# Kernel tuning notes

Hardware: AMD Instinct MI355X
Metric: run time of the kernel (lower is better)

The kernel has to match this reference:

```python
import jax, jax.numpy as jnp
import numpy as np
from jax import lax

B, C, N = 4, 512, 4096
NH = 8
HD = C // NH          # 64
SR = 2                # sr_ratio
EPS = 1e-5            # BatchNorm eps (torch default)


def setup_inputs() -> dict:
    key = jax.random.key(0)
    ks = jax.random.split(key, 12)
    d = {}
    d["x"] = jax.random.normal(ks[0], (B, C, N), jnp.float32)
    d["y"] = jax.random.normal(ks[1], (B, C, N), jnp.float32)  # unused by forward (faithful to source)
    # Conv1d kernel-size-1 weights == (out_c, in_c) matrices; trunc_normal std=0.02 ~ normal*0.02
    d["Wq"] = jax.random.normal(ks[2], (C, C), jnp.float32) * 0.02
    d["Wk"] = jax.random.normal(ks[3], (C, C), jnp.float32) * 0.02
    # sr: Conv2d(dim, dim, kernel=SR, stride=SR), kaiming-ish init per _init_weights
    fan_out = SR * SR * C
    d["Wsr"] = jax.random.normal(ks[4], (C, C, SR, SR), jnp.float32) * np.sqrt(2.0 / fan_out)
    d["bsr"] = jnp.zeros((C,), jnp.float32)
    # BatchNorm1d(dim) in inference mode
    d["bn_gamma"] = 1.0 + 0.1 * jax.random.normal(ks[5], (C,), jnp.float32)
    d["bn_beta"] = 0.1 * jax.random.normal(ks[6], (C,), jnp.float32)
    d["bn_mean"] = 0.1 * jax.random.normal(ks[7], (C,), jnp.float32)
    d["bn_var"] = 1.0 + 0.1 * jnp.abs(jax.random.normal(ks[8], (C,), jnp.float32))
    d["Wproj"] = jax.random.normal(ks[9], (C, C), jnp.float32) * 0.02
    d["bproj"] = jnp.zeros((C,), jnp.float32)
    d["H"] = 64
    d["W"] = 64
    return d


def reference(x, y, Wq, Wk, Wsr, bsr, bn_gamma, bn_beta, bn_mean, bn_var, Wproj, bproj, H, W):
    scale = HD ** -0.5
    # q: Conv1d(k=1) -> (B,C,N) -> (B,NH,HD,N) -> (B,NH,N,HD)
    q = jnp.einsum('oc,bcn->bon', Wq, x).reshape(B, NH, HD, N).transpose(0, 1, 3, 2)
    # spatial reduction path (sr_ratio > 1): Conv2d stride SR, then BN (inference), then k-proj
    x4 = x.reshape(B, C, H, W)
    xsr = lax.conv_general_dilated(x4, Wsr, (SR, SR), 'VALID',
                                   dimension_numbers=('NCHW', 'OIHW', 'NCHW'))
    xsr = xsr + bsr[None, :, None, None]
    xsr = xsr.reshape(B, C, -1)  # (B, C, Nk), Nk = (H//SR)*(W//SR)
    inv_std = lax.rsqrt(bn_var + EPS)
    xsr = (xsr - bn_mean[None, :, None]) * (inv_std * bn_gamma)[None, :, None] + bn_beta[None, :, None]
    k = jnp.einsum('oc,bcn->bon', Wk, xsr).reshape(B, NH, HD, -1)  # (B,NH,HD,Nk)
    # v: mean over tokens, replicated per head -> effectively (B, C)
    v = jnp.mean(x, axis=2)  # (B, C)
    # scores + max over keys (no softmax)
    attn = jnp.einsum('bhnd,bhdk->bhnk', q, k) * scale  # (B,NH,N,Nk)
    attn = jnp.max(attn, axis=-1)                        # (B,NH,N)
    # out[b,c,n] = sum_h attn[b,h,n] * v[b,c]  (attn^T @ v, then transpose)
    out = jnp.sum(attn, axis=1)[:, None, :] * v[:, :, None]  # (B,C,N)
    out = jnp.einsum('oc,bcn->bon', Wproj, out) + bproj[None, :, None]
    return out
```

## Files before the change

### kernel.cpp

```cpp
#include <hip/hip_runtime.h>
#include <hip/hip_bf16.h>

constexpr int B_ = 4, C_ = 512, N_ = 4096, NH_ = 8, HD_ = 64;
constexpr int NK = 1024;
constexpr float SCALE = 0.125f;
constexpr float EPS = 1e-5f;

typedef __attribute__((ext_vector_type(8))) short bf16x8;
typedef __attribute__((ext_vector_type(4))) float f32x4;

__device__ __forceinline__ short bf16s(float f) {
    __hip_bfloat16 h = __float2bfloat16(f);
    return *reinterpret_cast<short*>(&h);
}
__device__ __forceinline__ float bf2f(short s) {
    return __bfloat162float(*reinterpret_cast<__hip_bfloat16*>(&s));
}

#define GLD16(gp, lp)                                                                     \
    __builtin_amdgcn_global_load_lds((const __attribute__((address_space(1))) void*)(gp), \
                                     (__attribute__((address_space(3))) void*)(lp), 16, 0, 0)

__global__ __launch_bounds__(256) void k_xw(const float* __restrict__ x,
                                            const float* __restrict__ Wq, const float* __restrict__ Wk,
                                            const float* __restrict__ gamma, const float* __restrict__ beta,
                                            const float* __restrict__ mean, const float* __restrict__ var,
                                            const float* __restrict__ bsr, const float* __restrict__ Wsr,
                                            short* __restrict__ xT, float* __restrict__ vpart,
                                            short* __restrict__ Wq16, short* __restrict__ Wkp16,
                                            float* __restrict__ bk, short* __restrict__ WsrT) {
    const int bid = blockIdx.x, tid = threadIdx.x;
    __shared__ float t[64][65];
    if (bid < 2048) {
        const int y = bid & 63, ct = (bid >> 6) & 7, b = bid >> 9;
        {
            const int cc = tid >> 2, q = tid & 3;
            const float* xr = x + ((size_t)(b * C_ + ct * 64 + cc)) * N_ + y * 64;
            float s = 0.f;
#pragma unroll
            for (int jj = 0; jj < 4; ++jj) {
                float4 f = *reinterpret_cast<const float4*>(&xr[q * 16 + jj * 4]);
                int n = q * 16 + jj * 4;
                t[n + 0][cc] = f.x; t[n + 1][cc] = f.y;
                t[n + 2][cc] = f.z; t[n + 3][cc] = f.w;
                s += f.x + f.y + f.z + f.w;
            }
            s += __shfl_xor(s, 1);
            s += __shfl_xor(s, 2);
            if (q == 0) vpart[((size_t)(y * B_ + b)) * C_ + ct * 64 + cc] = s;
        }
        __syncthreads();
        {
            const int n = tid >> 2, c0 = (tid & 3) * 16;
            bf16x8 u0, u1;
#pragma unroll
            for (int j = 0; j < 8; ++j) {
                u0[j] = bf16s(t[n][c0 + j]);
                u1[j] = bf16s(t[n][c0 + 8 + j]);
            }
            short* dst = xT + ((size_t)(b * N_ + y * 64 + n)) * C_ + ct * 64 + c0;
            *reinterpret_cast<bf16x8*>(dst) = u0;
            *reinterpret_cast<bf16x8*>(dst + 8) = u1;
        }
    } else if (bid < 2560) {
        const int o = bid - 2048;
        float acc = 0.f;
        for (int c = tid; c < C_; c += 256) {
            float sc = rsqrtf(var[c] + EPS) * gamma[c];
            float wk = Wk[o * C_ + c];
            Wkp16[o * C_ + c] = bf16s(wk * sc);
            Wq16[o * C_ + c] = bf16s(Wq[o * C_ + c]);
            acc += wk * (sc * (bsr[c] - mean[c]) + beta[c]);
        }
        for (int m = 32; m; m >>= 1) acc += __shfl_xor(acc, m);
        if ((tid & 63) == 0) t[0][tid >> 6] = acc;
        __syncthreads();
        if (tid == 0) bk[o] = t[0][0] + t[0][1] + t[0][2] + t[0][3];
    } else {
        const int r = bid - 2560, kt = r & 31, ot = r >> 5;
        {
            const int cc = tid >> 2, q = tid & 3;
            const float* xr = Wsr + (size_t)(ot * 64 + cc) * 2048 + kt * 64;
#pragma unroll
            for (int jj = 0; jj < 4; ++jj) {
                float4 f = *reinterpret_cast<const float4*>(&xr[q * 16 + jj * 4]);
                int n = q * 16 + jj * 4;
                t[n + 0][cc] = f.x; t[n + 1][cc] = f.y;
                t[n + 2][cc] = f.z; t[n + 3][cc] = f.w;
            }
        }
        __syncthreads();
        {
            const int n = tid >> 2, c0 = (tid & 3) * 16;
            bf16x8 u0, u1;
#pragma unroll
            for (int j = 0; j < 8; ++j) {
                u0[j] = bf16s(t[n][c0 + j]);
                u1[j] = bf16s(t[n][c0 + 8 + j]);
            }
            int gkk = kt * 64 + n;
            int row2 = (gkk & 3) * 512 + (gkk >> 2);
            short* dst = WsrT + (size_t)row2 * C_ + ot * 64 + c0;
            *reinterpret_cast<bf16x8*>(dst) = u0;
            *reinterpret_cast<bf16x8*>(dst + 8) = u1;
        }
    }
}

template <int MT>
__device__ __forceinline__ void gemm_core(const short* __restrict__ Ag,
                                          const short* __restrict__ Bg, int K,
                                          short* Abuf, short* Bbuf,
                                          f32x4 (&acc)[MT][4]) {
    const int tid = threadIdx.x;
    const int w = tid >> 6, l = tid & 63;
    const int lr = l & 15, lg = l >> 4;
    const int wm = w >> 1, wn = w & 1;
    const int srow = tid >> 3, scol = (tid & 7) * 8;
    char* AbufC = (char*)Abuf;
    char* BbufC = (char*)Bbuf;
    for (int kt = 0; kt < K; kt += 64) {
#pragma unroll
        for (int i = 0; i < MT; ++i)
            GLD16(Ag + (size_t)(i * 32 + srow) * K + kt + scol, AbufC + i * 4096 + tid * 16);
#pragma unroll
        for (int i = 0; i < 4; ++i)
            GLD16(Bg + (size_t)(i * 32 + srow) * K + kt + scol, BbufC + i * 4096 + tid * 16);
        __syncthreads();
        bf16x8 af[MT][2], bfv[4][2];
#pragma unroll
        for (int mt = 0; mt < MT; ++mt)
#pragma unroll
            for (int ks = 0; ks < 2; ++ks)
                af[mt][ks] = *reinterpret_cast<const bf16x8*>(
                    &Abuf[(wm * MT * 16 + mt * 16 + lr) * 64 + ks * 32 + lg * 8]);
#pragma unroll
        for (int nt = 0; nt < 4; ++nt)
#pragma unroll
            for (int ks = 0; ks < 2; ++ks)
                bfv[nt][ks] = *reinterpret_cast<const bf16x8*>(
                    &Bbuf[(wn * 64 + nt * 16 + lr) * 64 + ks * 32 + lg * 8]);
#pragma unroll
        for (int mt = 0; mt < MT; ++mt)
#pragma unroll
            for (int nt = 0; nt < 4; ++nt) {
                acc[mt][nt] = __builtin_amdgcn_mfma_f32_16x16x32_bf16(af[mt][0], bfv[nt][0], acc[mt][nt], 0, 0, 0);
                acc[mt][nt] = __builtin_amdgcn_mfma_f32_16x16x32_bf16(af[mt][1], bfv[nt][1], acc[mt][nt], 0, 0, 0);
            }
        __syncthreads();
    }
}

__global__ __launch_bounds__(256) void k_gemm_wck(const short* __restrict__ Wkp16,
                                                  const short* __restrict__ WsrT,
                                                  short* __restrict__ Wck16) {
    __shared__ short Abuf[2 * 32 * 64];
    __shared__ short Bbuf[128 * 64];
    f32x4 acc[2][4];
#pragma unroll
    for (int i = 0; i < 2; ++i)
#pragma unroll
        for (int j = 0; j < 4; ++j) acc[i][j] = (f32x4){0.f, 0.f, 0.f, 0.f};
    const int m0 = blockIdx.y * 64, n0 = blockIdx.x * 128;
    gemm_core<2>(Wkp16 + (size_t)m0 * 512, WsrT + (size_t)n0 * 512, 512, Abuf, Bbuf, acc);
    const int tid = threadIdx.x, l = tid & 63, w = tid >> 6;
    const int lr = l & 15, lg = l >> 4, wm = w >> 1, wn = w & 1;
#pragma unroll
    for (int mt = 0; mt < 2; ++mt)
#pragma unroll
        for (int nt = 0; nt < 4; ++nt) {
            int kk = n0 + wn * 64 + nt * 16 + lr;
#pragma unroll
            for (int r = 0; r < 4; ++r) {
                int o = m0 + wm * 32 + mt * 16 + lg * 4 + r;
                Wck16[(size_t)o * 2048 + kk] = bf16s(acc[mt][nt][r]);
            }
        }
}

__global__ __launch_bounds__(256) void k_gemm_qk2(const short* __restrict__ xT,
                                                  const short* __restrict__ Wq16,
                                                  const short* __restrict__ Wck16,
                                                  short* __restrict__ kp,
                                                  short* __restrict__ q2) {
    __shared__ short Abuf[128 * 64];
    __shared__ short Bbuf[128 * 64];
    f32x4 acc[4][4];
#pragma unroll
    for (int i = 0; i < 4; ++i)
#pragma unroll
        for (int j = 0; j < 4; ++j) acc[i][j] = (f32x4){0.f, 0.f, 0.f, 0.f};
    const int bid = blockIdx.x;
    const int tid = threadIdx.x, l = tid & 63, w = tid >> 6;
    const int lr = l & 15, lg = l >> 4, wm = w >> 1, wn = w & 1;
    const int srow = tid >> 3, scol = (tid & 7) * 8;
    char* AbufC = (char*)Abuf;
    char* BbufC = (char*)Bbuf;

    if (bid < 256) {
        const int s = bid >> 7;
        const int r2 = bid & 127;
        const int n0 = (r2 >> 2) * 128;
        const int m0 = (r2 & 3) * 128;
        for (int kt2 = 0; kt2 < 1024; kt2 += 64) {
            const int dx = kt2 >> 9, cc = kt2 & 511;
#pragma unroll
            for (int i = 0; i < 4; ++i) {
                int bp = n0 + i * 32 + srow;
                int b = bp >> 10, p = bp & 1023;
                int n = ((p >> 5) * 2 + s) * 64 + (p & 31) * 2 + dx;
                GLD16(xT + ((size_t)(b * N_ + n)) * C_ + cc + scol, AbufC + i * 4096 + tid * 16);
            }
#pragma unroll
            for (int i = 0; i < 4; ++i)
                GLD16(Wck16 + (size_t)(m0 + i * 32 + srow) * 2048 + s * 1024 + kt2 + scol,
                      BbufC + i * 4096 + tid * 16);
            __syncthreads();
            bf16x8 af[4][2], bfv[4][2];
#pragma unroll
            for (int mt = 0; mt < 4; ++mt)
#pragma unroll
                for (int ks = 0; ks < 2; ++ks)
                    af[mt][ks] = *reinterpret_cast<const bf16x8*>(
                        &Abuf[(wm * 64 + mt * 16 + lr) * 64 + ks * 32 + lg * 8]);
#pragma unroll
            for (int nt = 0; nt < 4; ++nt)
#pragma unroll
                for (int ks = 0; ks < 2; ++ks)
                    bfv[nt][ks] = *reinterpret_cast<const bf16x8*>(
                        &Bbuf[(wn * 64 + nt * 16 + lr) * 64 + ks * 32 + lg * 8]);
#pragma unroll
            for (int mt = 0; mt < 4; ++mt)
#pragma unroll
                for (int nt = 0; nt < 4; ++nt) {
                    acc[mt][nt] = __builtin_amdgcn_mfma_f32_16x16x32_bf16(af[mt][0], bfv[nt][0], acc[mt][nt], 0, 0, 0);
                    acc[mt][nt] = __builtin_amdgcn_mfma_f32_16x16x32_bf16(af[mt][1], bfv[nt][1], acc[mt][nt], 0, 0, 0);
                }
            __syncthreads();
        }
        short* kps = kp + (size_t)s * (4096 * 512);
#pragma unroll
        for (int mt = 0; mt < 4; ++mt)
#pragma unroll
            for (int nt = 0; nt < 4; ++nt) {
                int o = m0 + wn * 64 + nt * 16 + lr;
#pragma unroll
                for (int r = 0; r < 4; ++r) {
                    int bp = n0 + wm * 64 + mt * 16 + lg * 4 + r;
                    kps[(size_t)bp * 512 + o] = bf16s(acc[mt][nt][r]);
                }
            }
    } else {
        const int bq = bid - 256;
        const int m0 = (bq & 3) * 128, n0 = (bq >> 2) * 128;
        gemm_core<4>(Wq16 + (size_t)m0 * 512, xT + (size_t)n0 * 512, 512, Abuf, Bbuf, acc);
#pragma unroll
        for (int mt = 0; mt < 4; ++mt) {
            const int o0 = m0 + wm * 64 + mt * 16 + lg * 4;
            const int h = o0 >> 6, d0 = o0 & 63;
#pragma unroll
            for (int nt = 0; nt < 4; ++nt) {
                int ng = n0 + wn * 64 + nt * 16 + lr;
                int b = ng >> 12, n = ng & 4095;
                short4 u;
                u.x = bf16s(acc[mt][nt][0]);
                u.y = bf16s(acc[mt][nt][1]);
                u.z = bf16s(acc[mt][nt][2]);
                u.w = bf16s(acc[mt][nt][3]);
                *reinterpret_cast<short4*>(&q2[(((size_t)(b * NH_ + h)) * N_ + n) * HD_ + d0]) = u;
            }
        }
    }
}

__global__ __launch_bounds__(256) void k_kredpv(const short* __restrict__ kp,
                                                const float* __restrict__ bk,
                                                const float* __restrict__ vpart,
                                                const float* __restrict__ Wproj,
                                                short* __restrict__ k3,
                                                float* __restrict__ pv) {
    const int bid = blockIdx.x, tid = threadIdx.x;
    if (bid < 4096) {
        const int bp = bid, b = bp >> 10, p = bp & 1023;
        const int o = tid * 2;
        const short* k0 = kp + (size_t)bp * 512 + o;
        short2 s0 = *reinterpret_cast<const short2*>(k0);
        short2 s1 = *reinterpret_cast<const short2*>(k0 + (size_t)4096 * 512);
        float2 bb = *reinterpret_cast<const float2*>(&bk[o]);
        short2 u;
        u.x = bf16s(bf2f(s0.x) + bf2f(s1.x) + bb.x);
        u.y = bf16s(bf2f(s0.y) + bf2f(s1.y) + bb.y);
        const int h = o >> 6, d = o & 63;
        *reinterpret_cast<short2*>(&k3[(((size_t)(b * NH_ + h)) * NK + p) * HD_ + d]) = u;
    } else {
        const int r = bid - 4096, oc = r & 7, b = r >> 3;
        __shared__ float vs[512];
        float2 s = {0.f, 0.f};
        for (int y = 0; y < 64; ++y) {
            float2 f = *reinterpret_cast<const float2*>(&vpart[((size_t)(y * B_ + b)) * C_ + tid * 2]);
            s.x += f.x; s.y += f.y;
        }
        vs[tid * 2] = s.x * (1.f / N_);
        vs[tid * 2 + 1] = s.y * (1.f / N_);
        __syncthreads();
        const int w = tid >> 6, l = tid & 63;
#pragma unroll 4
        for (int i = 0; i < 16; ++i) {
            int o = oc * 64 + i * 4 + w;
            const float* wr = Wproj + (size_t)o * C_;
            float4 a = *reinterpret_cast<const float4*>(&wr[l * 8]);
            float4 b4 = *reinterpret_cast<const float4*>(&wr[l * 8 + 4]);
            float acc = a.x * vs[l * 8] + a.y * vs[l * 8 + 1] + a.z * vs[l * 8 + 2] + a.w * vs[l * 8 + 3] +
                        b4.x * vs[l * 8 + 4] + b4.y * vs[l * 8 + 5] + b4.z * vs[l * 8 + 6] + b4.w * vs[l * 8 + 7];
            for (int m = 32; m; m >>= 1) acc += __shfl_xor(acc, m);
            if (l == 0) pv[b * C_ + o] = acc;
        }
    }
}

__global__ __launch_bounds__(256) void k_attn3(const short* __restrict__ k3,
                                               const short* __restrict__ q2,
                                               float* __restrict__ am) {
    const int b = blockIdx.z, h = blockIdx.y, n0 = blockIdx.x * 256;
    const int w = threadIdx.x >> 6, l = threadIdx.x & 63;
    const int lr = l & 15, lg = l >> 4;
    const short* qb = q2 + ((size_t)(b * NH_ + h)) * N_ * HD_;
    const short* kb = k3 + ((size_t)(b * NH_ + h)) * NK * HD_;

    bf16x8 bq[16][2];
#pragma unroll
    for (int nt = 0; nt < 16; ++nt)
#pragma unroll
        for (int ks = 0; ks < 2; ++ks)
            bq[nt][ks] = *reinterpret_cast<const bf16x8*>(
                &qb[(size_t)(n0 + nt * 16 + lr) * HD_ + ks * 32 + lg * 8]);

    float rmax[16];
#pragma unroll
    for (int nt = 0; nt < 16; ++nt) rmax[nt] = -3.4e38f;

    const short* kw = kb + (size_t)(w * 256) * HD_;
    const short* s0 = kw + (size_t)lr * HD_ + lg * 8;
    bf16x8 a0 = *reinterpret_cast<const bf16x8*>(s0);
    bf16x8 a1 = *reinterpret_cast<const bf16x8*>(s0 + 32);
    for (int t = 0; t < 16; ++t) {
        bf16x8 c0 = a0, c1 = a1;
        if (t < 15) {
            const short* s2 = kw + (size_t)((t + 1) * 16 + lr) * HD_ + lg * 8;
            a0 = *reinterpret_cast<const bf16x8*>(s2);
            a1 = *reinterpret_cast<const bf16x8*>(s2 + 32);
        }
        __builtin_amdgcn_s_setprio(1);
#pragma unroll
        for (int nt = 0; nt < 16; ++nt) {
            f32x4 acc = {0.f, 0.f, 0.f, 0.f};
            acc = __builtin_amdgcn_mfma_f32_16x16x32_bf16(c0, bq[nt][0], acc, 0, 0, 0);
            acc = __builtin_amdgcn_mfma_f32_16x16x32_bf16(c1, bq[nt][1], acc, 0, 0, 0);
            rmax[nt] = fmaxf(fmaxf(fmaxf(fmaxf(acc[0], acc[1]), acc[2]), acc[3]), rmax[nt]);
        }
        __builtin_amdgcn_s_setprio(0);
    }
#pragma unroll
    for (int nt = 0; nt < 16; ++nt) {
        float m = rmax[nt];
        m = fmaxf(m, __shfl_xor(m, 16));
        m = fmaxf(m, __shfl_xor(m, 32));
        rmax[nt] = m;
    }
    __shared__ float sm[4][256];
    if (lg == 0) {
#pragma unroll
        for (int nt = 0; nt < 16; ++nt) sm[w][nt * 16 + lr] = rmax[nt];
    }
    __syncthreads();
    {
        const int tid = threadIdx.x;
        float m = fmaxf(fmaxf(sm[0][tid], sm[1][tid]),
                        fmaxf(sm[2][tid], sm[3][tid]));
        am[((size_t)(b * NH_ + h)) * N_ + n0 + tid] = SCALE * m;
    }
}

__global__ __launch_bounds__(256) void k_final(const float* __restrict__ pv, const float* __restrict__ am,
                                               const float* __restrict__ bproj, float* __restrict__ out) {
    const int b = blockIdx.z, o0 = blockIdx.y * 64;
    const int n = blockIdx.x * 256 + (threadIdx.x & 63) * 4;
    const int og = threadIdx.x >> 6;
    float4 s = {0.f, 0.f, 0.f, 0.f};
#pragma unroll
    for (int h = 0; h < NH_; ++h) {
        float4 a = *reinterpret_cast<const float4*>(&am[((size_t)(b * NH_ + h)) * N_ + n]);
        s.x += a.x; s.y += a.y; s.z += a.z; s.w += a.w;
    }
    float* ob = out + (size_t)b * C_ * N_ + n;
    const float* pvb = pv + b * C_;
#pragma unroll 4
    for (int i = 0; i < 16; ++i) {
        int o = o0 + og * 16 + i;
        float p = pvb[o], bp = bproj[o];
        float4 r = {p * s.x + bp, p * s.y + bp, p * s.z + bp, p * s.w + bp};
        *reinterpret_cast<float4*>(&ob[(size_t)o * N_]) = r;
    }
}

extern "C" void kernel_launch(void* const* d_in, const int* in_sizes, int n_in,
                              void* d_out, int out_size, void* d_ws, size_t ws_size,
                              hipStream_t stream) {
    const float* x     = (const float*)d_in[0];
    const float* Wq    = (const float*)d_in[2];
    const float* Wk    = (const float*)d_in[3];
    const float* Wsr   = (const float*)d_in[4];
    const float* bsr   = (const float*)d_in[5];
    const float* gamma = (const float*)d_in[6];
    const float* beta  = (const float*)d_in[7];
    const float* mean  = (const float*)d_in[8];
    const float* var   = (const float*)d_in[9];
    const float* Wproj = (const float*)d_in[10];
    const float* bproj = (const float*)d_in[11];
    float* out = (float*)d_out;

    char* ws = (char*)d_ws;
    float* vpart = (float*)(ws + 0);
    float* pv    = (float*)(ws + 524288);
    float* bk    = (float*)(ws + 532480);
    float* am    = (float*)(ws + 536576);
    short* Wq16  = (short*)(ws + 1060864);
    short* Wkp16 = (short*)(ws + 1585152);
    short* WsrT  = (short*)(ws + 2109440);
    short* Wck16 = (short*)(ws + 4206592);
    short* xT    = (short*)(ws + 6303744);
    short* q2    = (short*)(ws + 23080960);
    short* k3    = (short*)(ws + 39858176);
    short* kp    = (short*)(ws + 44052480);

    k_xw<<<dim3(2816), 256, 0, stream>>>(x, Wq, Wk, gamma, beta, mean, var, bsr, Wsr,
                                         xT, vpart, Wq16, Wkp16, bk, WsrT);
    k_gemm_wck<<<dim3(16, 8), 256, 0, stream>>>(Wkp16, WsrT, Wck16);
    k_gemm_qk2<<<dim3(768), 256, 0, stream>>>(xT, Wq16, Wck16, kp, q2);
    k_kredpv<<<dim3(4128), 256, 0, stream>>>(kp, bk, vpart, Wproj, k3, pv);
    k_attn3<<<dim3(16, NH_, B_), 256, 0, stream>>>(k3, q2, am);
    k_final<<<dim3(16, 8, B_), 256, 0, stream>>>(pv, am, bproj, out);
}
```

Before: 107.4 us.

## Split fused sr-conv K GEMM into four partial sums and retile Wck and final kernels

The K-projection GEMM inside k_gemm_qk2 changes from a 2-way split with a 1024-long reduction to a 4-way split (one per conv tap dy,dx) with a 512-long reduction, giving 512 K blocks instead of 256. k_kredpv now sums four partials instead of two. The Wck GEMM is rewritten as a 64x64-tiled kernel with more blocks and vectorized short4 stores. k_final now launches more blocks, each doing 8 output rows. The aim is more parallelism and shorter serial reduction loops, paid for with double the partial-K buffer traffic (four bf16 slices of kp instead of two).

```diff
diff --git a/kernel.cpp b/kernel.cpp
--- a/kernel.cpp
+++ b/kernel.cpp
@@ -151,30 +151,64 @@
     }
 }
 
-__global__ __launch_bounds__(256) void k_gemm_wck(const short* __restrict__ Wkp16,
-                                                  const short* __restrict__ WsrT,
-                                                  short* __restrict__ Wck16) {
-    __shared__ short Abuf[2 * 32 * 64];
-    __shared__ short Bbuf[128 * 64];
-    f32x4 acc[2][4];
+__global__ __launch_bounds__(256) void k_wck64(const short* __restrict__ WsrT,
+                                               const short* __restrict__ Wkp16,
+                                               short* __restrict__ Wck16) {
+    __shared__ short Ab[64 * 64];
+    __shared__ short Bb[64 * 64];
+    const int m0 = blockIdx.x * 64;
+    const int n0 = blockIdx.y * 64;
+    const int tid = threadIdx.x, w = tid >> 6, l = tid & 63;
+    const int lr = l & 15, lg = l >> 4, wm = w >> 1, wn = w & 1;
+    const int srow = tid >> 3, scol = (tid & 7) * 8;
+    f32x4 acc[2][2];
 #pragma unroll
     for (int i = 0; i < 2; ++i)
 #pragma unroll
-        for (int j = 0; j < 4; ++j) acc[i][j] = (f32x4){0.f, 0.f, 0.f, 0.f};
-    const int m0 = blockIdx.y * 64, n0 = blockIdx.x * 128;
-    gemm_core<2>(Wkp16 + (size_t)m0 * 512, WsrT + (size_t)n0 * 512, 512, Abuf, Bbuf, acc);
-    const int tid = threadIdx.x, l = tid & 63, w = tid >> 6;
-    const int lr = l & 15, lg = l >> 4, wm = w >> 1, wn = w & 1;
+        for (int j = 0; j < 2; ++j) acc[i][j] = (f32x4){0.f, 0.f, 0.f, 0.f};
+    char* AbC = (char*)Ab;
+    char* BbC = (char*)Bb;
+    for (int kt = 0; kt < 512; kt += 64) {
+#pragma unroll
+        for (int j = 0; j < 2; ++j) {
+            GLD16(WsrT + (size_t)(m0 + j * 32 + srow) * 512 + kt + scol, AbC + j * 4096 + tid * 16);
+            GLD16(Wkp16 + (size_t)(n0 + j * 32 + srow) * 512 + kt + scol, BbC + j * 4096 + tid * 16);
+        }
+        __syncthreads();
+        bf16x8 af[2][2], bfv[2][2];
+#pragma unroll
+        for (int mt = 0; mt < 2; ++mt)
+#pragma unroll
+            for (int ks = 0; ks < 2; ++ks)
+                af[mt][ks] = *reinterpret_cast<const bf16x8*>(
+                    &Ab[(wm * 32 + mt * 16 + lr) * 64 + ks * 32 + lg * 8]);
+#pragma unroll
+        for (int nt = 0; nt < 2; ++nt)
+#pragma unroll
+            for (int ks = 0; ks < 2; ++ks)
+                bfv[nt][ks] = *reinterpret_cast<const bf16x8*>(
+                    &Bb[(wn * 32 + nt * 16 + lr) * 64 + ks * 32 + lg * 8]);
+#pragma unroll
+        for (int mt = 0; mt < 2; ++mt)
+#pragma unroll
+            for (int nt = 0; nt < 2; ++nt) {
+                acc[mt][nt] = __builtin_amdgcn_mfma_f32_16x16x32_bf16(af[mt][0], bfv[nt][0], acc[mt][nt], 0, 0, 0);
+                acc[mt][nt] = __builtin_amdgcn_mfma_f32_16x16x32_bf16(af[mt][1], bfv[nt][1], acc[mt][nt], 0, 0, 0);
+            }
+        __syncthreads();
+    }
 #pragma unroll
     for (int mt = 0; mt < 2; ++mt)
 #pragma unroll
-        for (int nt = 0; nt < 4; ++nt) {
-            int kk = n0 + wn * 64 + nt * 16 + lr;
-#pragma unroll
-            for (int r = 0; r < 4; ++r) {
-                int o = m0 + wm * 32 + mt * 16 + lg * 4 + r;
-                Wck16[(size_t)o * 2048 + kk] = bf16s(acc[mt][nt][r]);
-            }
+        for (int nt = 0; nt < 2; ++nt) {
+            int kk0 = m0 + wm * 32 + mt * 16 + lg * 4;
+            int o = n0 + wn * 32 + nt * 16 + lr;
+            short4 u;
+            u.x = bf16s(acc[mt][nt][0]);
+            u.y = bf16s(acc[mt][nt][1]);
+            u.z = bf16s(acc[mt][nt][2]);
+            u.w = bf16s(acc[mt][nt][3]);
+            *reinterpret_cast<short4*>(&Wck16[(size_t)o * 2048 + kk0]) = u;
         }
 }
 
@@ -197,23 +231,23 @@
     char* AbufC = (char*)Abuf;
     char* BbufC = (char*)Bbuf;
 
-    if (bid < 256) {
+    if (bid < 512) {
         const int s = bid >> 7;
+        const int dy = s >> 1, dx = s & 1;
         const int r2 = bid & 127;
         const int n0 = (r2 >> 2) * 128;
         const int m0 = (r2 & 3) * 128;
-        for (int kt2 = 0; kt2 < 1024; kt2 += 64) {
-            const int dx = kt2 >> 9, cc = kt2 & 511;
+        for (int kt2 = 0; kt2 < 512; kt2 += 64) {
 #pragma unroll
             for (int i = 0; i < 4; ++i) {
                 int bp = n0 + i * 32 + srow;
                 int b = bp >> 10, p = bp & 1023;
-                int n = ((p >> 5) * 2 + s) * 64 + (p & 31) * 2 + dx;
-                GLD16(xT + ((size_t)(b * N_ + n)) * C_ + cc + scol, AbufC + i * 4096 + tid * 16);
+                int n = ((p >> 5) * 2 + dy) * 64 + (p & 31) * 2 + dx;
+                GLD16(xT + ((size_t)(b * N_ + n)) * C_ + kt2 + scol, AbufC + i * 4096 + tid * 16);
             }
 #pragma unroll
             for (int i = 0; i < 4; ++i)
-                GLD16(Wck16 + (size_t)(m0 + i * 32 + srow) * 2048 + s * 1024 + kt2 + scol,
+                GLD16(Wck16 + (size_t)(m0 + i * 32 + srow) * 2048 + s * 512 + kt2 + scol,
                       BbufC + i * 4096 + tid * 16);
             __syncthreads();
             bf16x8 af[4][2], bfv[4][2];
@@ -251,7 +285,7 @@
                 }
             }
     } else {
-        const int bq = bid - 256;
+        const int bq = bid - 512;
         const int m0 = (bq & 3) * 128, n0 = (bq >> 2) * 128;
         gemm_core<4>(Wq16 + (size_t)m0 * 512, xT + (size_t)n0 * 512, 512, Abuf, Bbuf, acc);
 #pragma unroll
@@ -284,12 +318,17 @@
         const int bp = bid, b = bp >> 10, p = bp & 1023;
         const int o = tid * 2;
         const short* k0 = kp + (size_t)bp * 512 + o;
-        short2 s0 = *reinterpret_cast<const short2*>(k0);
-        short2 s1 = *reinterpret_cast<const short2*>(k0 + (size_t)4096 * 512);
         float2 bb = *reinterpret_cast<const float2*>(&bk[o]);
+        float sx = bb.x, sy = bb.y;
+#pragma unroll
+        for (int s = 0; s < 4; ++s) {
+            short2 v2 = *reinterpret_cast<const short2*>(k0 + (size_t)s * (4096 * 512));
+            sx += bf2f(v2.x);
+            sy += bf2f(v2.y);
+        }
         short2 u;
-        u.x = bf16s(bf2f(s0.x) + bf2f(s1.x) + bb.x);
-        u.y = bf16s(bf2f(s0.y) + bf2f(s1.y) + bb.y);
+        u.x = bf16s(sx);
+        u.y = bf16s(sy);
         const int h = o >> 6, d = o & 63;
         *reinterpret_cast<short2*>(&k3[(((size_t)(b * NH_ + h)) * NK + p) * HD_ + d]) = u;
     } else {
@@ -383,9 +422,8 @@
 
 __global__ __launch_bounds__(256) void k_final(const float* __restrict__ pv, const float* __restrict__ am,
                                                const float* __restrict__ bproj, float* __restrict__ out) {
-    const int b = blockIdx.z, o0 = blockIdx.y * 64;
-    const int n = blockIdx.x * 256 + (threadIdx.x & 63) * 4;
-    const int og = threadIdx.x >> 6;
+    const int b = blockIdx.z, o0 = blockIdx.y * 64 + (threadIdx.x >> 5) * 8;
+    const int n = blockIdx.x * 128 + (threadIdx.x & 31) * 4;
     float4 s = {0.f, 0.f, 0.f, 0.f};
 #pragma unroll
     for (int h = 0; h < NH_; ++h) {
@@ -394,9 +432,9 @@
     }
     float* ob = out + (size_t)b * C_ * N_ + n;
     const float* pvb = pv + b * C_;
-#pragma unroll 4
-    for (int i = 0; i < 16; ++i) {
-        int o = o0 + og * 16 + i;
+#pragma unroll
+    for (int i = 0; i < 8; ++i) {
+        int o = o0 + i;
         float p = pvb[o], bp = bproj[o];
         float4 r = {p * s.x + bp, p * s.y + bp, p * s.z + bp, p * s.w + bp};
         *reinterpret_cast<float4*>(&ob[(size_t)o * N_]) = r;
@@ -435,9 +473,9 @@
 
     k_xw<<<dim3(2816), 256, 0, stream>>>(x, Wq, Wk, gamma, beta, mean, var, bsr, Wsr,
                                          xT, vpart, Wq16, Wkp16, bk, WsrT);
-    k_gemm_wck<<<dim3(16, 8), 256, 0, stream>>>(Wkp16, WsrT, Wck16);
-    k_gemm_qk2<<<dim3(768), 256, 0, stream>>>(xT, Wq16, Wck16, kp, q2);
+    k_wck64<<<dim3(32, 8), 256, 0, stream>>>(WsrT, Wkp16, Wck16);
+    k_gemm_qk2<<<dim3(1024), 256, 0, stream>>>(xT, Wq16, Wck16, kp, q2);
     k_kredpv<<<dim3(4128), 256, 0, stream>>>(kp, bk, vpart, Wproj, k3, pv);
     k_attn3<<<dim3(16, NH_, B_), 256, 0, stream>>>(k3, q2, am);
-    k_final<<<dim3(16, 8, B_), 256, 0, stream>>>(pv, am, bproj, out);
-}
+    k_final<<<dim3(32, 8, B_), 256, 0, stream>>>(pv, am, bproj, out);
+}
```

Measured after the change: 101.8 us. -5.2%, faster.
